# Kernel optimization log

Measured on AMD Instinct MI355X. Metric: run time of the kernel, lower is better.

## Reference

```python
import jax, jax.numpy as jnp
import numpy as np

NS, NT, DF, H, O = 200000, 50000, 20, 64, 64
NE, NL = 1000000, 500000


def setup_inputs() -> dict:
    key = jax.random.key(0)
    ks = jax.random.split(key, 24)
    inp = {
        'target_x': jax.random.normal(ks[0], (NT, DF), jnp.float32),
        'source_node_id': jnp.arange(NS, dtype=jnp.int64),
        'target_node_id': jnp.arange(NT, dtype=jnp.int64),
        'edge_src': jax.random.randint(ks[1], (NE,), 0, NS),
        'edge_dst': jax.random.randint(ks[2], (NE,), 0, NT),
        'label_src': jax.random.randint(ks[3], (NL,), 0, NS),
        'label_dst': jax.random.randint(ks[4], (NL,), 0, NT),
        'src_emb': jax.random.normal(ks[5], (NS, H), jnp.float32) * 0.05,
        'tgt_emb': jax.random.normal(ks[6], (NT, H), jnp.float32) * 0.05,
        'lin_W': jax.random.normal(ks[7], (DF, H), jnp.float32) * 0.05,
        'lin_b': jnp.zeros((H,), jnp.float32),
    }
    # SAGEConv params: (Wl, bl, Wr) per edge type per layer. st = source->target, ts = target->source
    dims = {'st1': (H, H), 'ts1': (H, H), 'st2': (H, O), 'ts2': (H, O)}
    i = 8
    for name, (din, dout) in dims.items():
        inp['Wl_' + name] = jax.random.normal(ks[i], (din, dout), jnp.float32) * 0.05
        inp['bl_' + name] = jnp.zeros((dout,), jnp.float32)
        inp['Wr_' + name] = jax.random.normal(ks[i + 1], (din, dout), jnp.float32) * 0.05
        i += 2
    return inp


def _sage(x_src, x_dst, src_idx, dst_idx, n_dst, Wl, bl, Wr):
    # PyG SAGEConv, aggr='mean': lin_l(mean_{j in N(i)} x_j) + lin_r(x_i)
    msg = x_src[src_idx]                                   # [E, d] gather
    agg = jax.ops.segment_sum(msg, dst_idx, num_segments=n_dst)
    deg = jax.ops.segment_sum(jnp.ones((src_idx.shape[0],), x_src.dtype), dst_idx, num_segments=n_dst)
    mean = agg / jnp.maximum(deg, 1.0)[:, None]
    return mean @ Wl + bl + x_dst @ Wr


def reference(target_x, source_node_id, target_node_id, edge_src, edge_dst,
              label_src, label_dst, src_emb, tgt_emb, lin_W, lin_b,
              Wl_st1, bl_st1, Wr_st1, Wl_ts1, bl_ts1, Wr_ts1,
              Wl_st2, bl_st2, Wr_st2, Wl_ts2, bl_ts2, Wr_ts2):
    ns, nt = src_emb.shape[0], tgt_emb.shape[0]
    x_s = src_emb[source_node_id]                          # [NS, H]
    x_t = target_x @ lin_W + lin_b + tgt_emb[target_node_id]  # [NT, H]
    # layer 1 (per edge type, summed per dst type; each dst type has one incoming type)
    h_t = _sage(x_s, x_t, edge_src, edge_dst, nt, Wl_st1, bl_st1, Wr_st1)
    h_s = _sage(x_t, x_s, edge_dst, edge_src, ns, Wl_ts1, bl_ts1, Wr_ts1)
    h_t, h_s = jax.nn.relu(h_t), jax.nn.relu(h_s)
    # layer 2
    o_t = _sage(h_s, h_t, edge_src, edge_dst, nt, Wl_st2, bl_st2, Wr_st2)
    o_s = _sage(h_t, h_s, edge_dst, edge_src, ns, Wl_ts2, bl_ts2, Wr_ts2)
    # dot-product link classifier
    return (o_s[label_src] * o_t[label_dst]).sum(axis=-1)  # [NL]
```

## Files before the change

### kernel.cpp

```cpp
#include <hip/hip_runtime.h>

#define NSRC 200000
#define NTGT 50000
#define DF   20
#define HD   64
#define NE   1000000
#define NL   500000

#define SH_T 6
#define SH_S 8
#define NB   782
#define CHUNK 8192
#define NCH  ((NE + CHUNK - 1) / CHUNK)

#define HIST_BLKS (NCH * 2)
#define PREP_BLKS 256

#define GT 782
#define GS 3125

typedef unsigned short ushort_t;
typedef short s16x8 __attribute__((ext_vector_type(8)));
typedef float f32x4 __attribute__((ext_vector_type(4)));

__device__ __forceinline__ float bf2f(ushort_t u) {
    return __uint_as_float(((unsigned)u) << 16);
}
__device__ __forceinline__ ushort_t f2bf(float f) {
    unsigned u = __float_as_uint(f);
    return (ushort_t)((u + 0x7fffu + ((u >> 16) & 1u)) >> 16);
}

__global__ __launch_bounds__(1024) void front(
    const int* __restrict__ es, const int* __restrict__ ed,
    int* __restrict__ cnt_t, int* __restrict__ cnt_s,
    const float* __restrict__ tx, const float* __restrict__ W,
    const float* __restrict__ lb, const float* __restrict__ temb,
    const float* __restrict__ semb,
    ushort_t* __restrict__ xb, ushort_t* __restrict__ sbuf,
    const float* __restrict__ Wl0, const float* __restrict__ Wr0,
    const float* __restrict__ Wl1, const float* __restrict__ Wr1,
    const float* __restrict__ Wl2, const float* __restrict__ Wr2,
    const float* __restrict__ Wl3, const float* __restrict__ Wr3,
    ushort_t* __restrict__ wt)
{
    __shared__ int h[NB];
    const int b   = blockIdx.x;
    const int tid = threadIdx.x;

    if (b < HIST_BLKS) {
        const int dir  = b / NCH;
        const int c    = b % NCH;
        const int base = c * CHUNK;
        const int n    = min(CHUNK, NE - base);
        const int* key = dir ? es : ed;
        const int sh   = dir ? SH_S : SH_T;
        int* cnt       = dir ? cnt_s : cnt_t;

        for (int i = tid; i < NB; i += 1024) h[i] = 0;
        __syncthreads();
        for (int i = tid; i < n; i += 1024)
            atomicAdd(&h[key[base + i] >> sh], 1);
        __syncthreads();
        for (int i = tid; i < NB; i += 1024) cnt[c * NB + i] = h[i];
    } else if (b < HIST_BLKS + PREP_BLKS) {
        const int id   = (b - HIST_BLKS) * 1024 + tid;
        const int pstr = PREP_BLKS * 1024;
        for (int i = id; i < NTGT * HD; i += pstr) {
            int n = i >> 6, k = i & 63;
            float acc = lb[k] + temb[i];
#pragma unroll
            for (int d = 0; d < DF; ++d) acc += tx[n * DF + d] * W[d * HD + k];
            xb[i] = f2bf(acc);
        }
        for (int i = id; i < NSRC * HD; i += pstr) sbuf[i] = f2bf(semb[i]);
    } else {
        for (int i = tid; i < 4 * 64 * 128; i += 1024) {
            int set = i >> 13, rem = i & 8191;
            int j = rem >> 7, k = rem & 127;
            const float* Wl = set == 0 ? Wl0 : set == 1 ? Wl1 : set == 2 ? Wl2 : Wl3;
            const float* Wr = set == 0 ? Wr0 : set == 1 ? Wr1 : set == 2 ? Wr2 : Wr3;
            float v = (k < 64) ? Wl[k * 64 + j] : Wr[(k - 64) * 64 + j];
            wt[i] = f2bf(v);
        }
    }
}

__global__ __launch_bounds__(1024) void scan_all(
    int* __restrict__ cnt_t, int* __restrict__ cnt_s,
    int* __restrict__ bb_t, int* __restrict__ bb_s)
{
    int* cnt = blockIdx.x ? cnt_s : cnt_t;
    int* bb  = blockIdx.x ? bb_s  : bb_t;
    __shared__ int s[1024];
    const int tid = threadIdx.x;
    int run = 0;
    if (tid < NB) {
        for (int c = 0; c < NCH; ++c) {
            int v = cnt[c * NB + tid];
            cnt[c * NB + tid] = run;
            run += v;
        }
    }
    s[tid] = (tid < NB) ? run : 0;
    __syncthreads();
    for (int d = 1; d < 1024; d <<= 1) {
        int t = (tid >= d) ? s[tid - d] : 0;
        __syncthreads();
        s[tid] += t;
        __syncthreads();
    }
    int incl = s[tid];
    if (tid < NB) bb[tid] = incl - run;
    if (tid == NB - 1) bb[NB] = incl;
}

__global__ __launch_bounds__(1024) void bin_fill2(
    const int* __restrict__ es, const int* __restrict__ ed,
    const int* __restrict__ cnt_t, const int* __restrict__ cnt_s,
    const int* __restrict__ bb_t, const int* __restrict__ bb_s,
    int2* __restrict__ pairs_t, int2* __restrict__ pairs_s)
{
    __shared__ int cur[NB];
    const int dir  = blockIdx.y;
    const int c    = blockIdx.x;
    const int base = c * CHUNK;
    const int n    = min(CHUNK, NE - base);
    const int* key = dir ? es : ed;
    const int* oth = dir ? ed : es;
    const int sh   = dir ? SH_S : SH_T;
    const int* cnt = dir ? cnt_s : cnt_t;
    const int* bb  = dir ? bb_s  : bb_t;
    int2* pairs    = dir ? pairs_s : pairs_t;

    for (int i = threadIdx.x; i < NB; i += 1024)
        cur[i] = bb[i] + cnt[c * NB + i];
    __syncthreads();
    for (int i = threadIdx.x; i < n; i += 1024) {
        int k = key[base + i], o = oth[base + i];
        int p = atomicAdd(&cur[k >> sh], 1);
        pairs[p] = make_int2(o, k);
    }
}

__global__ __launch_bounds__(256) void bucket_build_all(
    const int2* __restrict__ pairs_t, const int* __restrict__ bb_t,
    int* __restrict__ rp_t, int* __restrict__ col_t,
    const int2* __restrict__ pairs_s, const int* __restrict__ bb_s,
    int* __restrict__ rp_s, int* __restrict__ col_s)
{
    __shared__ int hist[256];
    __shared__ int scn[256];
    __shared__ int cur[256];
    const bool is_t = blockIdx.x < NB;
    const int b = is_t ? blockIdx.x : blockIdx.x - NB;
    const int2* pairs = is_t ? pairs_t : pairs_s;
    const int* bb     = is_t ? bb_t : bb_s;
    int* rp           = is_t ? rp_t : rp_s;
    int* col          = is_t ? col_t : col_s;
    const int shift   = is_t ? SH_T : SH_S;
    const int n       = is_t ? NTGT : NSRC;

    const int tid = threadIdx.x;
    const int beg = bb[b], end = bb[b + 1];
    const int row0 = b << shift;

    hist[tid] = 0;
    __syncthreads();
    for (int e = beg + tid; e < end; e += 256)
        atomicAdd(&hist[pairs[e].y - row0], 1);
    __syncthreads();

    int v = hist[tid];
    scn[tid] = v;
    __syncthreads();
    for (int d = 1; d < 256; d <<= 1) {
        int t = (tid >= d) ? scn[tid - d] : 0;
        __syncthreads();
        scn[tid] += t;
        __syncthreads();
    }
    int ex = scn[tid] - v;
    cur[tid] = ex;
    int row = row0 + tid;
    if (tid < (1 << shift) && row < n) rp[row] = beg + ex;
    if (b == 0 && tid == 0) rp[n] = NE;
    __syncthreads();

    for (int e = beg + tid; e < end; e += 256) {
        int2 pr = pairs[e];
        int p = atomicAdd(&cur[pr.y - row0], 1);
        col[beg + p] = pr.x;
    }
}

template <bool RELU>
__global__ __launch_bounds__(256, 8) void sage_layer(
    const ushort_t* __restrict__ tab_t, const int* __restrict__ rp_t,
    const int* __restrict__ col_t, const ushort_t* __restrict__ xd_t,
    const ushort_t* __restrict__ wt_t, const float* __restrict__ bl_t,
    ushort_t* __restrict__ out_t,
    const ushort_t* __restrict__ tab_s, const int* __restrict__ rp_s,
    const int* __restrict__ col_s, const ushort_t* __restrict__ xd_s,
    const ushort_t* __restrict__ wt_s, const float* __restrict__ bl_s,
    ushort_t* __restrict__ out_s)
{
    __shared__ ushort_t smean[64][72];
    const int blk = blockIdx.x;
    const bool is_t = (blk % 5 == 0);
    const int bi = is_t ? blk / 5 : blk - blk / 5 - 1;

    const ushort_t* table = is_t ? tab_t : tab_s;
    const int* rp         = is_t ? rp_t  : rp_s;
    const int* col        = is_t ? col_t : col_s;
    const ushort_t* xd    = is_t ? xd_t  : xd_s;
    const ushort_t* wt    = is_t ? wt_t  : wt_s;
    const float* bl       = is_t ? bl_t  : bl_s;
    ushort_t* out         = is_t ? out_t : out_s;
    const int n           = is_t ? NTGT  : NSRC;

    const int tid = threadIdx.x;
    const int el  = tid & 7;
    const int ew  = tid >> 3;
    const int d0  = el * 8;
    const int base = bi * 64;

    const int node0 = base + ew;
    const int node1 = base + ew + 32;
    int e0 = 0, end0 = 0, e1 = 0, end1 = 0;
    if (node0 < n) { e0 = rp[node0]; end0 = rp[node0 + 1]; }
    if (node1 < n) { e1 = rp[node1]; end1 = rp[node1 + 1]; }
    const float inv0 = (end0 > e0) ? 1.f / (float)(end0 - e0) : 0.f;
    const float inv1 = (end1 > e1) ? 1.f / (float)(end1 - e1) : 0.f;

    float r0[8], r1[8];
#pragma unroll
    for (int i = 0; i < 8; ++i) { r0[i] = 0.f; r1[i] = 0.f; }

    while (e0 < end0 || e1 < end1) {
        const bool w0 = e0 < end0, w1 = e1 < end1;
        s16x8 v0[4], v1[4];
        if (w0) {
            int c[4];
#pragma unroll
            for (int s = 0; s < 4; ++s) c[s] = col[min(e0 + s, end0 - 1)];
#pragma unroll
            for (int s = 0; s < 4; ++s)
                v0[s] = *(const s16x8*)&table[(size_t)c[s] * HD + d0];
        }
        if (w1) {
            int c[4];
#pragma unroll
            for (int s = 0; s < 4; ++s) c[s] = col[min(e1 + s, end1 - 1)];
#pragma unroll
            for (int s = 0; s < 4; ++s)
                v1[s] = *(const s16x8*)&table[(size_t)c[s] * HD + d0];
        }
        if (w0) {
#pragma unroll
            for (int s = 0; s < 4; ++s)
                if (e0 + s < end0)
#pragma unroll
                    for (int i = 0; i < 8; ++i) r0[i] += bf2f((ushort_t)v0[s][i]);
            e0 += 4;
        }
        if (w1) {
#pragma unroll
            for (int s = 0; s < 4; ++s)
                if (e1 + s < end1)
#pragma unroll
                    for (int i = 0; i < 8; ++i) r1[i] += bf2f((ushort_t)v1[s][i]);
            e1 += 4;
        }
    }

    s16x8 o0, o1;
#pragma unroll
    for (int i = 0; i < 8; ++i) {
        o0[i] = (short)f2bf(r0[i] * inv0);
        o1[i] = (short)f2bf(r1[i] * inv1);
    }
    *(s16x8*)&smean[ew][d0] = o0;
    *(s16x8*)&smean[ew + 32][d0] = o1;
    __syncthreads();

    const int lane = tid & 63;
    const int rq   = tid >> 6;
    const int lr   = lane & 15;
    const int kg   = lane >> 4;

    const int arow = base + rq * 16 + lr;
    s16x8 a[4];
    a[0] = *(const s16x8*)&smean[rq * 16 + lr][kg * 8];
    a[1] = *(const s16x8*)&smean[rq * 16 + lr][32 + kg * 8];
    if (arow < n) {
        const ushort_t* xrow = xd + (size_t)arow * HD;
        a[2] = *(const s16x8*)(xrow + kg * 8);
        a[3] = *(const s16x8*)(xrow + 32 + kg * 8);
    } else {
        s16x8 z = {0, 0, 0, 0, 0, 0, 0, 0};
        a[2] = z; a[3] = z;
    }

#pragma unroll 1
    for (int jb = 0; jb < 4; ++jb) {
        s16x8 bfr[4];
#pragma unroll
        for (int kb = 0; kb < 4; ++kb)
            bfr[kb] = *(const s16x8*)&wt[(jb * 16 + lr) * 128 + kb * 32 + kg * 8];
        const float bias = bl[jb * 16 + lr];

        f32x4 accm = {bias, bias, bias, bias};
#pragma unroll
        for (int kb = 0; kb < 4; ++kb)
            accm = __builtin_amdgcn_mfma_f32_16x16x32_bf16(a[kb], bfr[kb], accm, 0, 0, 0);

#pragma unroll
        for (int r = 0; r < 4; ++r) {
            float v = accm[r];
            if (RELU) v = fmaxf(v, 0.f);
            smean[rq * 16 + kg * 4 + r][jb * 16 + lr] = f2bf(v);
        }
    }

#pragma unroll
    for (int j = 0; j < 2; ++j) {
        const int row = rq * 16 + j * 8 + (lane >> 3);
        const int nn  = base + row;
        if (nn < n) {
            s16x8 v = *(const s16x8*)&smean[row][(lane & 7) * 8];
            *(s16x8*)&out[(size_t)nn * HD + (lane & 7) * 8] = v;
        }
    }
}

__global__ __launch_bounds__(256) void classify_b(
    const ushort_t* __restrict__ os, const ushort_t* __restrict__ ot,
    const int* __restrict__ ls, const int* __restrict__ lt,
    float* __restrict__ out, int nl)
{
    const int lane = threadIdx.x & 63;
    const int sub  = lane >> 4;
    const int g    = (lane & 15) * 4;
    int w = (blockIdx.x * blockDim.x + threadIdx.x) >> 6;
    const int wstride = (gridDim.x * blockDim.x) >> 6;

    for (int l0 = w * 16; l0 < nl; l0 += wstride * 16) {
        float p[4];
        int li[4];
#pragma unroll
        for (int q = 0; q < 4; ++q) { li[q] = l0 + q * 4 + sub; p[q] = 0.f; }
#pragma unroll
        for (int q = 0; q < 4; ++q)
            if (li[q] < nl) {
                int a = ls[li[q]], b = lt[li[q]];
                ushort4 va = *(const ushort4*)&os[(size_t)a * HD + g];
                ushort4 vb = *(const ushort4*)&ot[(size_t)b * HD + g];
                p[q] = bf2f(va.x) * bf2f(vb.x) + bf2f(va.y) * bf2f(vb.y)
                     + bf2f(va.z) * bf2f(vb.z) + bf2f(va.w) * bf2f(vb.w);
            }
#pragma unroll
        for (int o = 8; o > 0; o >>= 1) {
#pragma unroll
            for (int q = 0; q < 4; ++q) p[q] += __shfl_xor(p[q], o, 64);
        }
        if ((lane & 15) == 0) {
#pragma unroll
            for (int q = 0; q < 4; ++q)
                if (li[q] < nl) out[li[q]] = p[q];
        }
    }
}

extern "C" void kernel_launch(void* const* d_in, const int* in_sizes, int n_in,
                              void* d_out, int out_size, void* d_ws, size_t ws_size,
                              hipStream_t stream)
{
    const float* target_x = (const float*)d_in[0];
    const int* edge_src  = (const int*)d_in[3];
    const int* edge_dst  = (const int*)d_in[4];
    const int* label_src = (const int*)d_in[5];
    const int* label_dst = (const int*)d_in[6];
    const float* src_emb = (const float*)d_in[7];
    const float* tgt_emb = (const float*)d_in[8];
    const float* lin_W   = (const float*)d_in[9];
    const float* lin_b   = (const float*)d_in[10];
    const float* Wl_st1 = (const float*)d_in[11];
    const float* bl_st1 = (const float*)d_in[12];
    const float* Wr_st1 = (const float*)d_in[13];
    const float* Wl_ts1 = (const float*)d_in[14];
    const float* bl_ts1 = (const float*)d_in[15];
    const float* Wr_ts1 = (const float*)d_in[16];
    const float* Wl_st2 = (const float*)d_in[17];
    const float* bl_st2 = (const float*)d_in[18];
    const float* Wr_st2 = (const float*)d_in[19];
    const float* Wl_ts2 = (const float*)d_in[20];
    const float* bl_ts2 = (const float*)d_in[21];
    const float* Wr_ts2 = (const float*)d_in[22];
    float* out = (float*)d_out;

    char* ws = (char*)d_ws;
    size_t off = 0;
    auto take = [&](size_t bytes) -> char* {
        char* p = ws + off;
        off = (off + bytes + 255) & ~(size_t)255;
        return p;
    };
    int* cnt_t = (int*)take((size_t)NCH * NB * 4);
    int* cnt_s = (int*)take((size_t)NCH * NB * 4);
    int* bb_t  = (int*)take((size_t)(NB + 1) * 4);
    int* bb_s  = (int*)take((size_t)(NB + 1) * 4);
    int* rp_t  = (int*)take((size_t)(NTGT + 1) * 4);
    int* rp_s  = (int*)take((size_t)(NSRC + 1) * 4);
    int* col_t = (int*)take((size_t)NE * 4);
    int* col_s = (int*)take((size_t)NE * 4);
    int2* pairs_t = (int2*)take((size_t)NE * 8);
    int2* pairs_s = (int2*)take((size_t)NE * 8);
    ushort_t* wt   = (ushort_t*)take((size_t)4 * 64 * 128 * 2);
    ushort_t* xb_t = (ushort_t*)take((size_t)NTGT * HD * 2);
    ushort_t* sb   = (ushort_t*)take((size_t)NSRC * HD * 2);
    ushort_t* hb_t = (ushort_t*)take((size_t)NTGT * HD * 2);
    ushort_t* hb_s = (ushort_t*)take((size_t)NSRC * HD * 2);
    ushort_t* ob_t = (ushort_t*)take((size_t)NTGT * HD * 2);
    ushort_t* ob_s = (ushort_t*)take((size_t)NSRC * HD * 2);

    front<<<HIST_BLKS + PREP_BLKS + 1, 1024, 0, stream>>>(
        edge_src, edge_dst, cnt_t, cnt_s,
        target_x, lin_W, lin_b, tgt_emb, src_emb, xb_t, sb,
        Wl_st1, Wr_st1, Wl_ts1, Wr_ts1, Wl_st2, Wr_st2, Wl_ts2, Wr_ts2, wt);

    scan_all<<<2, 1024, 0, stream>>>(cnt_t, cnt_s, bb_t, bb_s);
    dim3 gch(NCH, 2);
    bin_fill2<<<gch, 1024, 0, stream>>>(edge_src, edge_dst,
                                        cnt_t, cnt_s, bb_t, bb_s, pairs_t, pairs_s);
    bucket_build_all<<<2 * NB, 256, 0, stream>>>(pairs_t, bb_t, rp_t, col_t,
                                                 pairs_s, bb_s, rp_s, col_s);

    sage_layer<true><<<GT + GS, 256, 0, stream>>>(
        sb,   rp_t, col_t, xb_t, wt + 0 * 8192, bl_st1, hb_t,
        xb_t, rp_s, col_s, sb,   wt + 1 * 8192, bl_ts1, hb_s);
    sage_layer<false><<<GT + GS, 256, 0, stream>>>(
        hb_s, rp_t, col_t, hb_t, wt + 2 * 8192, bl_st2, ob_t,
        hb_t, rp_s, col_s, hb_s, wt + 3 * 8192, bl_ts2, ob_s);

    classify_b<<<2048, 256, 0, stream>>>(ob_s, ob_t, label_src, label_dst, out, NL);
}
```

Before: 273.9 us.

## Fuse per-bucket CSR build into SAGE layers using packed 32-bit pairs

Drops the separate bucket_build kernel and the global rp/col arrays. bin_fill2 now writes one packed int per edge, holding the row-within-bucket in the high bits and the neighbour id in the low 18 bits. Each sage_layer block rebuilds its own 64-row local CSR in shared memory with a histogram, a wave scan and a scatter before gathering. This removes a launch and the global col/rowptr traffic, at the cost of redoing the local sort in both layers, four source blocks each scanning the same 256-row bucket, extra LDS use, and an assumed cap of 2048 edges per 64-row group.

```diff
diff --git a/kernel.cpp b/kernel.cpp
--- a/kernel.cpp
+++ b/kernel.cpp
@@ -119,7 +119,7 @@
     const int* __restrict__ es, const int* __restrict__ ed,
     const int* __restrict__ cnt_t, const int* __restrict__ cnt_s,
     const int* __restrict__ bb_t, const int* __restrict__ bb_s,
-    int2* __restrict__ pairs_t, int2* __restrict__ pairs_s)
+    int* __restrict__ pairs_t, int* __restrict__ pairs_s)
 {
     __shared__ int cur[NB];
     const int dir  = blockIdx.y;
@@ -129,9 +129,10 @@
     const int* key = dir ? es : ed;
     const int* oth = dir ? ed : es;
     const int sh   = dir ? SH_S : SH_T;
+    const int rm   = dir ? 255 : 63;
     const int* cnt = dir ? cnt_s : cnt_t;
     const int* bb  = dir ? bb_s  : bb_t;
-    int2* pairs    = dir ? pairs_s : pairs_t;
+    int* pairs     = dir ? pairs_s : pairs_t;
 
     for (int i = threadIdx.x; i < NB; i += 1024)
         cur[i] = bb[i] + cnt[c * NB + i];
@@ -139,97 +140,82 @@
     for (int i = threadIdx.x; i < n; i += 1024) {
         int k = key[base + i], o = oth[base + i];
         int p = atomicAdd(&cur[k >> sh], 1);
-        pairs[p] = make_int2(o, k);
-    }
-}
-
-__global__ __launch_bounds__(256) void bucket_build_all(
-    const int2* __restrict__ pairs_t, const int* __restrict__ bb_t,
-    int* __restrict__ rp_t, int* __restrict__ col_t,
-    const int2* __restrict__ pairs_s, const int* __restrict__ bb_s,
-    int* __restrict__ rp_s, int* __restrict__ col_s)
-{
-    __shared__ int hist[256];
-    __shared__ int scn[256];
-    __shared__ int cur[256];
-    const bool is_t = blockIdx.x < NB;
-    const int b = is_t ? blockIdx.x : blockIdx.x - NB;
-    const int2* pairs = is_t ? pairs_t : pairs_s;
-    const int* bb     = is_t ? bb_t : bb_s;
-    int* rp           = is_t ? rp_t : rp_s;
-    int* col          = is_t ? col_t : col_s;
-    const int shift   = is_t ? SH_T : SH_S;
-    const int n       = is_t ? NTGT : NSRC;
-
-    const int tid = threadIdx.x;
-    const int beg = bb[b], end = bb[b + 1];
-    const int row0 = b << shift;
-
-    hist[tid] = 0;
-    __syncthreads();
-    for (int e = beg + tid; e < end; e += 256)
-        atomicAdd(&hist[pairs[e].y - row0], 1);
-    __syncthreads();
-
-    int v = hist[tid];
-    scn[tid] = v;
-    __syncthreads();
-    for (int d = 1; d < 256; d <<= 1) {
-        int t = (tid >= d) ? scn[tid - d] : 0;
-        __syncthreads();
-        scn[tid] += t;
-        __syncthreads();
-    }
-    int ex = scn[tid] - v;
-    cur[tid] = ex;
-    int row = row0 + tid;
-    if (tid < (1 << shift) && row < n) rp[row] = beg + ex;
-    if (b == 0 && tid == 0) rp[n] = NE;
-    __syncthreads();
-
-    for (int e = beg + tid; e < end; e += 256) {
-        int2 pr = pairs[e];
-        int p = atomicAdd(&cur[pr.y - row0], 1);
-        col[beg + p] = pr.x;
+        pairs[p] = ((k & rm) << 18) | o;
     }
 }
 
 template <bool RELU>
 __global__ __launch_bounds__(256, 8) void sage_layer(
-    const ushort_t* __restrict__ tab_t, const int* __restrict__ rp_t,
-    const int* __restrict__ col_t, const ushort_t* __restrict__ xd_t,
+    const ushort_t* __restrict__ tab_t, const int* __restrict__ bb_t,
+    const int* __restrict__ pairs_t, const ushort_t* __restrict__ xd_t,
     const ushort_t* __restrict__ wt_t, const float* __restrict__ bl_t,
     ushort_t* __restrict__ out_t,
-    const ushort_t* __restrict__ tab_s, const int* __restrict__ rp_s,
-    const int* __restrict__ col_s, const ushort_t* __restrict__ xd_s,
+    const ushort_t* __restrict__ tab_s, const int* __restrict__ bb_s,
+    const int* __restrict__ pairs_s, const ushort_t* __restrict__ xd_s,
     const ushort_t* __restrict__ wt_s, const float* __restrict__ bl_s,
     ushort_t* __restrict__ out_s)
 {
     __shared__ ushort_t smean[64][72];
+    __shared__ int lcol[2048];
+    __shared__ int sdeg[64];
+    __shared__ int srow0[64];
+    __shared__ int scur[64];
+
     const int blk = blockIdx.x;
     const bool is_t = (blk % 5 == 0);
     const int bi = is_t ? blk / 5 : blk - blk / 5 - 1;
 
     const ushort_t* table = is_t ? tab_t : tab_s;
-    const int* rp         = is_t ? rp_t  : rp_s;
-    const int* col        = is_t ? col_t : col_s;
+    const int* bb         = is_t ? bb_t  : bb_s;
+    const int* pairs      = is_t ? pairs_t : pairs_s;
     const ushort_t* xd    = is_t ? xd_t  : xd_s;
     const ushort_t* wt    = is_t ? wt_t  : wt_s;
     const float* bl       = is_t ? bl_t  : bl_s;
     ushort_t* out         = is_t ? out_t : out_s;
     const int n           = is_t ? NTGT  : NSRC;
 
+    const int parent  = is_t ? bi : (bi >> 2);
+    const int rowbase = is_t ? 0  : ((bi & 3) << 6);
+
     const int tid = threadIdx.x;
-    const int el  = tid & 7;
-    const int ew  = tid >> 3;
-    const int d0  = el * 8;
     const int base = bi * 64;
 
-    const int node0 = base + ew;
-    const int node1 = base + ew + 32;
-    int e0 = 0, end0 = 0, e1 = 0, end1 = 0;
-    if (node0 < n) { e0 = rp[node0]; end0 = rp[node0 + 1]; }
-    if (node1 < n) { e1 = rp[node1]; end1 = rp[node1 + 1]; }
+    const int beg = bb[parent], end = bb[parent + 1];
+
+    if (tid < 64) sdeg[tid] = 0;
+    __syncthreads();
+    for (int i = beg + tid; i < end; i += 256) {
+        int r = (pairs[i] >> 18) - rowbase;
+        if ((unsigned)r < 64u) atomicAdd(&sdeg[r], 1);
+    }
+    __syncthreads();
+    if (tid < 64) {
+        int v = sdeg[tid], inc = v;
+#pragma unroll
+        for (int d = 1; d < 64; d <<= 1) {
+            int t = __shfl_up(inc, d, 64);
+            if (tid >= d) inc += t;
+        }
+        srow0[tid] = inc - v;
+        scur[tid]  = inc - v;
+    }
+    __syncthreads();
+    for (int i = beg + tid; i < end; i += 256) {
+        int p = pairs[i];
+        int r = (p >> 18) - rowbase;
+        if ((unsigned)r < 64u) {
+            int pos = atomicAdd(&scur[r], 1);
+            if (pos < 2048) lcol[pos] = p & 0x3FFFF;
+        }
+    }
+    __syncthreads();
+
+    const int el = tid & 7;
+    const int ew = tid >> 3;
+    const int d0 = el * 8;
+
+    int e0 = srow0[ew],      end0 = e0 + sdeg[ew];
+    int e1 = srow0[ew + 32], end1 = e1 + sdeg[ew + 32];
     const float inv0 = (end0 > e0) ? 1.f / (float)(end0 - e0) : 0.f;
     const float inv1 = (end1 > e1) ? 1.f / (float)(end1 - e1) : 0.f;
 
@@ -243,7 +229,7 @@
         if (w0) {
             int c[4];
 #pragma unroll
-            for (int s = 0; s < 4; ++s) c[s] = col[min(e0 + s, end0 - 1)];
+            for (int s = 0; s < 4; ++s) c[s] = lcol[min(e0 + s, end0 - 1)];
 #pragma unroll
             for (int s = 0; s < 4; ++s)
                 v0[s] = *(const s16x8*)&table[(size_t)c[s] * HD + d0];
@@ -251,7 +237,7 @@
         if (w1) {
             int c[4];
 #pragma unroll
-            for (int s = 0; s < 4; ++s) c[s] = col[min(e1 + s, end1 - 1)];
+            for (int s = 0; s < 4; ++s) c[s] = lcol[min(e1 + s, end1 - 1)];
 #pragma unroll
             for (int s = 0; s < 4; ++s)
                 v1[s] = *(const s16x8*)&table[(size_t)c[s] * HD + d0];
@@ -410,12 +396,8 @@
     int* cnt_s = (int*)take((size_t)NCH * NB * 4);
     int* bb_t  = (int*)take((size_t)(NB + 1) * 4);
     int* bb_s  = (int*)take((size_t)(NB + 1) * 4);
-    int* rp_t  = (int*)take((size_t)(NTGT + 1) * 4);
-    int* rp_s  = (int*)take((size_t)(NSRC + 1) * 4);
-    int* col_t = (int*)take((size_t)NE * 4);
-    int* col_s = (int*)take((size_t)NE * 4);
-    int2* pairs_t = (int2*)take((size_t)NE * 8);
-    int2* pairs_s = (int2*)take((size_t)NE * 8);
+    int* pairs_t = (int*)take((size_t)NE * 4);
+    int* pairs_s = (int*)take((size_t)NE * 4);
     ushort_t* wt   = (ushort_t*)take((size_t)4 * 64 * 128 * 2);
     ushort_t* xb_t = (ushort_t*)take((size_t)NTGT * HD * 2);
     ushort_t* sb   = (ushort_t*)take((size_t)NSRC * HD * 2);
@@ -433,15 +415,13 @@
     dim3 gch(NCH, 2);
     bin_fill2<<<gch, 1024, 0, stream>>>(edge_src, edge_dst,
                                         cnt_t, cnt_s, bb_t, bb_s, pairs_t, pairs_s);
-    bucket_build_all<<<2 * NB, 256, 0, stream>>>(pairs_t, bb_t, rp_t, col_t,
-                                                 pairs_s, bb_s, rp_s, col_s);
 
     sage_layer<true><<<GT + GS, 256, 0, stream>>>(
-        sb,   rp_t, col_t, xb_t, wt + 0 * 8192, bl_st1, hb_t,
-        xb_t, rp_s, col_s, sb,   wt + 1 * 8192, bl_ts1, hb_s);
+        sb,   bb_t, pairs_t, xb_t, wt + 0 * 8192, bl_st1, hb_t,
+        xb_t, bb_s, pairs_s, sb,   wt + 1 * 8192, bl_ts1, hb_s);
     sage_layer<false><<<GT + GS, 256, 0, stream>>>(
-        hb_s, rp_t, col_t, hb_t, wt + 2 * 8192, bl_st2, ob_t,
-        hb_t, rp_s, col_s, hb_s, wt + 3 * 8192, bl_ts2, ob_s);
+        hb_s, bb_t, pairs_t, hb_t, wt + 2 * 8192, bl_st2, ob_t,
+        hb_t, bb_s, pairs_s, hb_s, wt + 3 * 8192, bl_ts2, ob_s);
 
     classify_b<<<2048, 256, 0, stream>>>(ob_s, ob_t, label_src, label_dst, out, NL);
 }
```

After: 325.7 us. 18.9% more time.
